# Performance work log

Hardware: AMD Instinct MI355X
Metric: run time of the kernel (lower is better)

The kernel has to match this reference:

```python
import jax, jax.numpy as jnp
import numpy as np

N = 50000   # nodes
E = 1600000 # edges (avg degree 32)
H = 128     # input_size == hidden_size
L = 2       # n_layer


def setup_inputs() -> dict:
    key = jax.random.key(0)
    k0, k1, k2, k3, k4 = jax.random.split(key, 5)
    inp = jax.random.normal(k0, (N, H), dtype=jnp.float32)
    h = jax.random.normal(k1, (L, N, H), dtype=jnp.float32)
    edgidx = jax.random.randint(k2, (2, E), 0, N, dtype=jnp.int32)
    # stacked gate linears, order per layer: xz, hz, xr, hr, xh, hh
    W = jax.random.normal(k3, (L, 6, H, H), dtype=jnp.float32) * (1.0 / np.sqrt(H))
    b = jax.random.normal(k4, (L, 6, H), dtype=jnp.float32) * 0.01
    return {"inp": inp, "edgidx": edgidx, "h": h, "W": W, "b": b}


def _gin(x, W, b, src, dst, n):
    # GINConv with eps=0: Linear(x + sum_{j in N(i)} x_j)
    agg = jax.ops.segment_sum(x[src], dst, num_segments=n)  # scatter-add over edges
    return (x + agg) @ W + b


def reference(inp, edgidx, h, W, b):
    src, dst = edgidx[0], edgidx[1]
    n = inp.shape[0]
    x = inp
    outs = []
    for i in range(W.shape[0]):  # small fixed layer loop
        z = jax.nn.sigmoid(_gin(x, W[i, 0], b[i, 0], src, dst, n)
                           + _gin(h[i], W[i, 1], b[i, 1], src, dst, n))
        r = jax.nn.sigmoid(_gin(x, W[i, 2], b[i, 2], src, dst, n)
                           + _gin(h[i], W[i, 3], b[i, 3], src, dst, n))
        h_tilde = jnp.tanh(_gin(x, W[i, 4], b[i, 4], src, dst, n)
                           + _gin(r * h[i], W[i, 5], b[i, 5], src, dst, n))
        x = z * h[i] + (1.0 - z) * h_tilde
        outs.append(x)
    h_out = jnp.stack(outs)  # [L, N, H]; original returns (out, h_out) where out is h_out
    return h_out
```

## Files before the change

### kernel.cpp

```cpp
#include <hip/hip_runtime.h>
#include <math.h>

#define HDIM 128

typedef _Float16 f16;
typedef unsigned short u16;
typedef __attribute__((ext_vector_type(4))) _Float16 f16x4;
typedef __attribute__((ext_vector_type(8))) _Float16 f16x8;
typedef __attribute__((ext_vector_type(4))) float f32x4;

__global__ __launch_bounds__(256) void degrank_kernel(
    const int* __restrict__ edg, int* __restrict__ cnt,
    u16* __restrict__ rank, int E) {
  int e = blockIdx.x * 256 + threadIdx.x;
  if (e < E) {
    int src = edg[e];
    int dst = edg[E + e];
    rank[e] = (u16)atomicAdd(&cnt[dst * 16 + (src >> 12)], 1);
  }
}

__global__ __launch_bounds__(256) void nodescan_kernel(
    int* __restrict__ cnt, int* __restrict__ deg, int N) {
  int node = blockIdx.x * 256 + threadIdx.x;
  if (node >= N) return;
  int* c = cnt + node * 16;
  int s = 0;
  #pragma unroll
  for (int b = 0; b < 16; ++b) {
    int v = c[b];
    c[b] = s;
    s += v;
  }
  deg[node] = s;
}

__global__ __launch_bounds__(256) void scan_part_kernel(
    const int* __restrict__ deg, int* __restrict__ bsum, int n, int chunk) {
  __shared__ int red[256];
  const int b = blockIdx.x, t = threadIdx.x;
  const int begin = b * chunk;
  const int end = min(begin + chunk, n);
  int s = 0;
  for (int i = begin + t; i < end; i += 256) s += deg[i];
  red[t] = s;
  __syncthreads();
  for (int off = 128; off > 0; off >>= 1) {
    if (t < off) red[t] += red[t + off];
    __syncthreads();
  }
  if (t == 0) bsum[b] = red[0];
}

__global__ __launch_bounds__(256) void scan_top_kernel(
    const int* __restrict__ bsum, int* __restrict__ boff,
    int* __restrict__ offs, int n) {
  __shared__ int sh[256];
  const int t = threadIdx.x;
  int v = bsum[t];
  sh[t] = v;
  __syncthreads();
  for (int off = 1; off < 256; off <<= 1) {
    int add = (t >= off) ? sh[t - off] : 0;
    __syncthreads();
    sh[t] += add;
    __syncthreads();
  }
  boff[t] = sh[t] - v;
  if (t == 255) offs[n] = sh[255];
}

__global__ __launch_bounds__(256) void scan_fin_kernel(
    const int* __restrict__ deg, const int* __restrict__ boff,
    int* __restrict__ offs, int n, int chunk) {
  __shared__ int sh[256];
  const int b = blockIdx.x, t = threadIdx.x;
  const int idx = b * chunk + t;
  int v = (t < chunk && idx < n) ? deg[idx] : 0;
  sh[t] = v;
  __syncthreads();
  for (int off = 1; off < 256; off <<= 1) {
    int add = (t >= off) ? sh[t - off] : 0;
    __syncthreads();
    sh[t] += add;
    __syncthreads();
  }
  if (t < chunk && idx < n) offs[idx] = boff[b] + sh[t] - v;
}

__global__ __launch_bounds__(256) void fill_kernel(
    const int* __restrict__ edg, const int* __restrict__ offs,
    const int* __restrict__ cnt, const u16* __restrict__ rank,
    u16* __restrict__ csr_src, int E) {
  int i = blockIdx.x * 256 + threadIdx.x;
  int e0 = i * 4;
  if (e0 >= E) return;
  if (e0 + 4 <= E) {
    int4 s4 = *reinterpret_cast<const int4*>(edg + e0);
    int4 d4 = *reinterpret_cast<const int4*>(edg + E + e0);
    ushort4 r4 = *reinterpret_cast<const ushort4*>(rank + e0);
    csr_src[offs[d4.x] + cnt[d4.x * 16 + (s4.x >> 12)] + r4.x] = (u16)s4.x;
    csr_src[offs[d4.y] + cnt[d4.y * 16 + (s4.y >> 12)] + r4.y] = (u16)s4.y;
    csr_src[offs[d4.z] + cnt[d4.z * 16 + (s4.z >> 12)] + r4.z] = (u16)s4.z;
    csr_src[offs[d4.w] + cnt[d4.w * 16 + (s4.w >> 12)] + r4.w] = (u16)s4.w;
  } else {
    for (int e = e0; e < E; ++e) {
      int src = edg[e];
      int dst = edg[E + e];
      csr_src[offs[dst] + cnt[dst * 16 + (src >> 12)] + rank[e]] = (u16)src;
    }
  }
}

__global__ __launch_bounds__(256) void convb_kernel(
    const float* __restrict__ src, f16* __restrict__ dst, int n, int SN) {
  const int t = threadIdx.x;
  const int nloc = t >> 3;
  const int sub = t & 7;
  const int sl = sub >> 1;
  const int hf = sub & 1;
  const int node = blockIdx.x * 32 + nloc;
  if (node >= n) return;
  const float* sp = src + (size_t)node * HDIM + sub * 16;
  f16* dp = dst + ((size_t)sl * SN + node) * 32 + hf * 16;
  float4 v0 = *reinterpret_cast<const float4*>(sp + 0);
  float4 v1 = *reinterpret_cast<const float4*>(sp + 4);
  float4 v2 = *reinterpret_cast<const float4*>(sp + 8);
  float4 v3 = *reinterpret_cast<const float4*>(sp + 12);
  f16x8 o0, o1;
  o0[0]=(f16)v0.x; o0[1]=(f16)v0.y; o0[2]=(f16)v0.z; o0[3]=(f16)v0.w;
  o0[4]=(f16)v1.x; o0[5]=(f16)v1.y; o0[6]=(f16)v1.z; o0[7]=(f16)v1.w;
  o1[0]=(f16)v2.x; o1[1]=(f16)v2.y; o1[2]=(f16)v2.z; o1[3]=(f16)v2.w;
  o1[4]=(f16)v3.x; o1[5]=(f16)v3.y; o1[6]=(f16)v3.z; o1[7]=(f16)v3.w;
  *reinterpret_cast<f16x8*>(dp) = o0;
  *reinterpret_cast<f16x8*>(dp + 8) = o1;
}

__global__ __launch_bounds__(256) void transw_kernel(
    const float* __restrict__ W, f16* __restrict__ WT) {
  __shared__ float sh[32][33];
  const int g = blockIdx.y;
  const int ti = blockIdx.x >> 2;
  const int tj = blockIdx.x & 3;
  const float* __restrict__ wp = W + (size_t)g * HDIM * HDIM;
  f16* __restrict__ op = WT + (size_t)g * HDIM * HDIM;
  const int t = threadIdx.x;
  #pragma unroll
  for (int it = 0; it < 4; ++it) {
    int elem = it * 256 + t;
    int r = elem >> 5, c = elem & 31;
    sh[r][c] = wp[(size_t)(ti * 32 + r) * HDIM + tj * 32 + c];
  }
  __syncthreads();
  #pragma unroll
  for (int it = 0; it < 4; ++it) {
    int elem = it * 256 + t;
    int cc = elem >> 5, rr = elem & 31;
    op[(size_t)(tj * 32 + cc) * HDIM + ti * 32 + rr] = (f16)sh[rr][cc];
  }
}

__global__ __launch_bounds__(256) void pull2_kernel(
    const u16* __restrict__ csr_src, const int* __restrict__ offs,
    const f16* __restrict__ xb, const f16* __restrict__ hbl,
    f16* __restrict__ A, f16* __restrict__ Bh, int N, int hSN) {
  const int cls = blockIdx.x & 7;
  const int tid = cls >> 2;
  const int sl = cls & 3;
  const int node = (blockIdx.x >> 3) * 64 + (threadIdx.x >> 2);
  if (node >= N) return;
  const int c8 = (threadIdx.x & 3) << 3;
  const f16* __restrict__ tab =
      tid ? hbl + (size_t)sl * hSN * 32 : xb + (size_t)sl * (size_t)N * 32;
  f16* __restrict__ dst = (tid ? Bh : A) + (size_t)sl * (size_t)N * 32;
  const int s = offs[node];
  const int e = offs[node + 1];
  float acc[8];
  f16x8 sv = *reinterpret_cast<const f16x8*>(tab + (size_t)node * 32 + c8);
  #pragma unroll
  for (int q = 0; q < 8; ++q) acc[q] = (float)sv[q];
  int k = s;
  for (; k + 8 <= e; k += 8) {
    int j0 = csr_src[k];
    int j1 = csr_src[k + 1];
    int j2 = csr_src[k + 2];
    int j3 = csr_src[k + 3];
    int j4 = csr_src[k + 4];
    int j5 = csr_src[k + 5];
    int j6 = csr_src[k + 6];
    int j7 = csr_src[k + 7];
    f16x8 u0 = *reinterpret_cast<const f16x8*>(tab + (size_t)j0 * 32 + c8);
    f16x8 u1 = *reinterpret_cast<const f16x8*>(tab + (size_t)j1 * 32 + c8);
    f16x8 u2 = *reinterpret_cast<const f16x8*>(tab + (size_t)j2 * 32 + c8);
    f16x8 u3 = *reinterpret_cast<const f16x8*>(tab + (size_t)j3 * 32 + c8);
    f16x8 u4 = *reinterpret_cast<const f16x8*>(tab + (size_t)j4 * 32 + c8);
    f16x8 u5 = *reinterpret_cast<const f16x8*>(tab + (size_t)j5 * 32 + c8);
    f16x8 u6 = *reinterpret_cast<const f16x8*>(tab + (size_t)j6 * 32 + c8);
    f16x8 u7 = *reinterpret_cast<const f16x8*>(tab + (size_t)j7 * 32 + c8);
    #pragma unroll
    for (int q = 0; q < 8; ++q)
      acc[q] += (((float)u0[q] + (float)u1[q]) + ((float)u2[q] + (float)u3[q])) +
                (((float)u4[q] + (float)u5[q]) + ((float)u6[q] + (float)u7[q]));
  }
  for (; k < e; ++k) {
    f16x8 u = *reinterpret_cast<const f16x8*>(tab + (size_t)csr_src[k] * 32 + c8);
    #pragma unroll
    for (int q = 0; q < 8; ++q) acc[q] += (float)u[q];
  }
  f16x8 o;
  #pragma unroll
  for (int q = 0; q < 8; ++q) o[q] = (f16)acc[q];
  *reinterpret_cast<f16x8*>(dst + (size_t)node * 32 + c8) = o;
}

__global__ __launch_bounds__(256) void pull1_kernel(
    const u16* __restrict__ csr_src, const int* __restrict__ offs,
    const f16* __restrict__ cb, f16* __restrict__ Ctot, int N) {
  const int sl = blockIdx.x & 3;
  const int node = (blockIdx.x >> 2) * 64 + (threadIdx.x >> 2);
  if (node >= N) return;
  const int c8 = (threadIdx.x & 3) << 3;
  const f16* __restrict__ tab = cb + (size_t)sl * (size_t)N * 32;
  f16* __restrict__ dst = Ctot + (size_t)sl * (size_t)N * 32;
  const int s = offs[node];
  const int e = offs[node + 1];
  float acc[8];
  f16x8 sv = *reinterpret_cast<const f16x8*>(tab + (size_t)node * 32 + c8);
  #pragma unroll
  for (int q = 0; q < 8; ++q) acc[q] = (float)sv[q];
  int k = s;
  for (; k + 8 <= e; k += 8) {
    int j0 = csr_src[k];
    int j1 = csr_src[k + 1];
    int j2 = csr_src[k + 2];
    int j3 = csr_src[k + 3];
    int j4 = csr_src[k + 4];
    int j5 = csr_src[k + 5];
    int j6 = csr_src[k + 6];
    int j7 = csr_src[k + 7];
    f16x8 u0 = *reinterpret_cast<const f16x8*>(tab + (size_t)j0 * 32 + c8);
    f16x8 u1 = *reinterpret_cast<const f16x8*>(tab + (size_t)j1 * 32 + c8);
    f16x8 u2 = *reinterpret_cast<const f16x8*>(tab + (size_t)j2 * 32 + c8);
    f16x8 u3 = *reinterpret_cast<const f16x8*>(tab + (size_t)j3 * 32 + c8);
    f16x8 u4 = *reinterpret_cast<const f16x8*>(tab + (size_t)j4 * 32 + c8);
    f16x8 u5 = *reinterpret_cast<const f16x8*>(tab + (size_t)j5 * 32 + c8);
    f16x8 u6 = *reinterpret_cast<const f16x8*>(tab + (size_t)j6 * 32 + c8);
    f16x8 u7 = *reinterpret_cast<const f16x8*>(tab + (size_t)j7 * 32 + c8);
    #pragma unroll
    for (int q = 0; q < 8; ++q)
      acc[q] += (((float)u0[q] + (float)u1[q]) + ((float)u2[q] + (float)u3[q])) +
                (((float)u4[q] + (float)u5[q]) + ((float)u6[q] + (float)u7[q]));
  }
  for (; k < e; ++k) {
    f16x8 u = *reinterpret_cast<const f16x8*>(tab + (size_t)csr_src[k] * 32 + c8);
    #pragma unroll
    for (int q = 0; q < 8; ++q) acc[q] += (float)u[q];
  }
  f16x8 o;
  #pragma unroll
  for (int q = 0; q < 8; ++q) o[q] = (f16)acc[q];
  *reinterpret_cast<f16x8*>(dst + (size_t)node * 32 + c8) = o;
}

__device__ __forceinline__ void stage_blocked(
    const f16* __restrict__ src, f16* __restrict__ As,
    int row0, int N, int SN, int t) {
  #pragma unroll
  for (int i = 0; i < 4; ++i) {
    int u = i * 256 + t;
    int row = u >> 4;
    int sl = (u >> 2) & 3;
    int ck = u & 3;
    int r = row0 + row;
    f16x8 v{};
    if (r < N) v = *reinterpret_cast<const f16x8*>(
        src + ((size_t)sl * SN + r) * 32 + ck * 8);
    *reinterpret_cast<f16x8*>(&As[row * 136 + sl * 32 + ck * 8]) = v;
  }
}

__device__ __forceinline__ void mfma_tile(
    const f16* As, const f16* Ws, int wr, int wc, int ln15, int quad,
    f32x4 (&acc)[2][4]) {
  #pragma unroll
  for (int s = 0; s < 4; ++s) {
    f16x8 a0 = *reinterpret_cast<const f16x8*>(
        &As[(wr * 32 + ln15) * 136 + s * 32 + quad * 8]);
    f16x8 a1 = *reinterpret_cast<const f16x8*>(
        &As[(wr * 32 + 16 + ln15) * 136 + s * 32 + quad * 8]);
    #pragma unroll
    for (int ni = 0; ni < 4; ++ni) {
      f16x8 bf = *reinterpret_cast<const f16x8*>(
          &Ws[(wc * 64 + ni * 16 + ln15) * 136 + s * 32 + quad * 8]);
      acc[0][ni] = __builtin_amdgcn_mfma_f32_16x16x32_f16(a0, bf, acc[0][ni], 0, 0, 0);
      acc[1][ni] = __builtin_amdgcn_mfma_f32_16x16x32_f16(a1, bf, acc[1][ni], 0, 0, 0);
    }
  }
}

__global__ __launch_bounds__(256, 3) void gemm3_kernel(
    const f16* __restrict__ A, const f16* __restrict__ Bh,
    const f16* __restrict__ WT, const float* __restrict__ b,
    const f16* __restrict__ hbl, f16* __restrict__ zb,
    f16* __restrict__ cb, float* __restrict__ hpre, int N, int hSN) {
  __shared__ f16 As[64 * 136];
  __shared__ f16 Ws[128 * 136];
  const int t = threadIdx.x;
  const int w = t >> 6, wr = w >> 1, wc = w & 1;
  const int lane = t & 63, ln15 = lane & 15, quad = lane >> 4;
  const int row0 = blockIdx.x * 64;
  f32x4 accZ[2][4], accR[2][4], accH[2][4];
  #pragma unroll
  for (int i = 0; i < 2; ++i)
    #pragma unroll
    for (int j = 0; j < 4; ++j) {
      accZ[i][j] = (f32x4){0.f, 0.f, 0.f, 0.f};
      accR[i][j] = (f32x4){0.f, 0.f, 0.f, 0.f};
      accH[i][j] = (f32x4){0.f, 0.f, 0.f, 0.f};
    }

  stage_blocked(A, As, row0, N, N, t);
  #pragma unroll
  for (int g = 0; g < 3; ++g) {
    const f16* __restrict__ wp = WT + (size_t)(g * 2) * HDIM * HDIM;
    __syncthreads();
    #pragma unroll
    for (int i = 0; i < 8; ++i) {
      int flat = i * 256 + t;
      int n = flat >> 4;
      int o = (flat & 15) * 8;
      *reinterpret_cast<f16x8*>(&Ws[n * 136 + o]) =
          *reinterpret_cast<const f16x8*>(wp + (size_t)n * HDIM + o);
    }
    __syncthreads();
    if (g == 0) mfma_tile(As, Ws, wr, wc, ln15, quad, accZ);
    else if (g == 1) mfma_tile(As, Ws, wr, wc, ln15, quad, accR);
    else mfma_tile(As, Ws, wr, wc, ln15, quad, accH);
  }
  __syncthreads();
  stage_blocked(Bh, As, row0, N, N, t);
  #pragma unroll
  for (int g = 0; g < 2; ++g) {
    const f16* __restrict__ wp = WT + (size_t)(g * 2 + 1) * HDIM * HDIM;
    __syncthreads();
    #pragma unroll
    for (int i = 0; i < 8; ++i) {
      int flat = i * 256 + t;
      int n = flat >> 4;
      int o = (flat & 15) * 8;
      *reinterpret_cast<f16x8*>(&Ws[n * 136 + o]) =
          *reinterpret_cast<const f16x8*>(wp + (size_t)n * HDIM + o);
    }
    __syncthreads();
    if (g == 0) mfma_tile(As, Ws, wr, wc, ln15, quad, accZ);
    else mfma_tile(As, Ws, wr, wc, ln15, quad, accR);
  }

  #pragma unroll
  for (int ni = 0; ni < 4; ++ni) {
    const int col = wc * 64 + ni * 16 + ln15;
    const int slc = col >> 5;
    const int cw = col & 31;
    float bz = b[0 * HDIM + col] + b[1 * HDIM + col];
    float br = b[2 * HDIM + col] + b[3 * HDIM + col];
    float bh = b[4 * HDIM + col];
    #pragma unroll
    for (int mi = 0; mi < 2; ++mi) {
      #pragma unroll
      for (int r = 0; r < 4; ++r) {
        int row = row0 + wr * 32 + mi * 16 + quad * 4 + r;
        if (row >= N) continue;
        size_t idx = (size_t)row * HDIM + col;
        zb[idx] = (f16)(accZ[mi][ni][r] + bz);
        float rv = accR[mi][ni][r] + br;
        float rg = 1.f / (1.f + expf(-rv));
        float hv = (float)hbl[((size_t)slc * hSN + row) * 32 + cw];
        cb[((size_t)slc * N + row) * 32 + cw] = (f16)(rg * hv);
        hpre[idx] = accH[mi][ni][r] + bh;
      }
    }
  }
}

__global__ __launch_bounds__(256, 3) void gemm_final_kernel(
    const f16* __restrict__ Ctot, const f16* __restrict__ WT5,
    const float* __restrict__ b5, const f16* __restrict__ zb,
    const float* __restrict__ hi, float* __restrict__ outi,
    f16* __restrict__ xb, int N) {
  __shared__ f16 As[64 * 136];
  __shared__ f16 Ws[128 * 136];
  const int t = threadIdx.x;
  const int w = t >> 6, wr = w >> 1, wc = w & 1;
  const int lane = t & 63, ln15 = lane & 15, quad = lane >> 4;
  const int row0 = blockIdx.x * 64;
  f32x4 acc[2][4];
  #pragma unroll
  for (int i = 0; i < 2; ++i)
    #pragma unroll
    for (int j = 0; j < 4; ++j) acc[i][j] = (f32x4){0.f, 0.f, 0.f, 0.f};

  stage_blocked(Ctot, As, row0, N, N, t);
  #pragma unroll
  for (int i = 0; i < 8; ++i) {
    int flat = i * 256 + t;
    int n = flat >> 4;
    int o = (flat & 15) * 8;
    *reinterpret_cast<f16x8*>(&Ws[n * 136 + o]) =
        *reinterpret_cast<const f16x8*>(WT5 + (size_t)n * HDIM + o);
  }
  __syncthreads();
  mfma_tile(As, Ws, wr, wc, ln15, quad, acc);

  #pragma unroll
  for (int ni = 0; ni < 4; ++ni) {
    const int col = wc * 64 + ni * 16 + ln15;
    const int slc = col >> 5;
    const int cw = col & 31;
    float bias = b5[col];
    #pragma unroll
    for (int mi = 0; mi < 2; ++mi) {
      #pragma unroll
      for (int r = 0; r < 4; ++r) {
        int row = row0 + wr * 32 + mi * 16 + quad * 4 + r;
        if (row >= N) continue;
        size_t idx = (size_t)row * HDIM + col;
        float v = acc[mi][ni][r] + bias + outi[idx];
        float ht = tanhf(v);
        float z = 1.f / (1.f + expf(-(float)zb[idx]));
        float o = z * hi[idx] + (1.f - z) * ht;
        outi[idx] = o;
        xb[((size_t)slc * N + row) * 32 + cw] = (f16)o;
      }
    }
  }
}

extern "C" void kernel_launch(void* const* d_in, const int* in_sizes, int n_in,
                              void* d_out, int out_size, void* d_ws, size_t ws_size,
                              hipStream_t stream) {
  const float* inp = (const float*)d_in[0];
  const int*   edg = (const int*)d_in[1];
  const float* h   = (const float*)d_in[2];
  const float* W   = (const float*)d_in[3];
  const float* b   = (const float*)d_in[4];
  float* out = (float*)d_out;

  const int NH = in_sizes[0];
  const int N  = NH / HDIM;
  const int E  = in_sizes[1] / 2;
  const int L  = in_sizes[2] / NH;

  f16* Af   = (f16*)d_ws;
  f16* Bhf  = Af + (size_t)NH;
  f16* zbuf = Bhf + (size_t)NH;
  f16* cbuf = zbuf + (size_t)NH;
  f16* xbuf = cbuf + (size_t)NH;
  f16* hbuf = xbuf + (size_t)NH;
  f16* WT   = hbuf + (size_t)L * NH;
  int* deg     = (int*)(WT + (size_t)L * 6 * HDIM * HDIM);
  int* offs    = deg + N;
  int* bsum    = offs + (N + 1);
  int* boff    = bsum + 256;
  u16* rank    = (u16*)(boff + 256);
  u16* csr_src = rank + (size_t)E;
  int* cnt     = (int*)Af;

  const int eblocks = (E + 255) / 256;
  const int fblocks = (E + 1023) / 1024;
  const int nsblocks = (N + 255) / 256;
  const int rowblocks = (N + 63) / 64;
  const int p2blocks = ((N + 63) / 64) * 8;
  const int p1blocks = ((N + 63) / 64) * 4;
  const int cvxblocks = (N + 31) / 32;
  const int cvhblocks = (L * N + 31) / 32;
  const int chunk = (N + 255) / 256;

  hipMemsetAsync(cnt, 0, (size_t)N * 16 * sizeof(int), stream);
  hipLaunchKernelGGL(degrank_kernel, dim3(eblocks), dim3(256), 0, stream,
                     edg, cnt, rank, E);
  hipLaunchKernelGGL(nodescan_kernel, dim3(nsblocks), dim3(256), 0, stream,
                     cnt, deg, N);
  hipLaunchKernelGGL(scan_part_kernel, dim3(256), dim3(256), 0, stream,
                     deg, bsum, N, chunk);
  hipLaunchKernelGGL(scan_top_kernel, dim3(1), dim3(256), 0, stream,
                     bsum, boff, offs, N);
  hipLaunchKernelGGL(scan_fin_kernel, dim3(256), dim3(256), 0, stream,
                     deg, boff, offs, N, chunk);
  hipLaunchKernelGGL(fill_kernel, dim3(fblocks), dim3(256), 0, stream,
                     edg, offs, cnt, rank, csr_src, E);
  hipLaunchKernelGGL(transw_kernel, dim3(16, L * 6), dim3(256), 0, stream,
                     W, WT);
  hipLaunchKernelGGL(convb_kernel, dim3(cvxblocks), dim3(256), 0, stream,
                     inp, xbuf, N, N);
  hipLaunchKernelGGL(convb_kernel, dim3(cvhblocks), dim3(256), 0, stream,
                     h, hbuf, L * N, L * N);

  for (int i = 0; i < L; ++i) {
    const float* hi = h + (size_t)i * NH;
    const f16* hbl = hbuf + (size_t)i * N * 32;
    const f16* WTi = WT + (size_t)i * 6 * HDIM * HDIM;
    const float* bi = b + (size_t)i * 6 * HDIM;
    float* outi = out + (size_t)i * NH;

    hipLaunchKernelGGL(pull2_kernel, dim3(p2blocks), dim3(256), 0, stream,
                       csr_src, offs, xbuf, hbl, Af, Bhf, N, L * N);
    hipLaunchKernelGGL(gemm3_kernel, dim3(rowblocks), dim3(256), 0, stream,
                       Af, Bhf, WTi, bi, hbl, zbuf, cbuf, outi, N, L * N);
    hipLaunchKernelGGL(pull1_kernel, dim3(p1blocks), dim3(256), 0, stream,
                       csr_src, offs, cbuf, Af, N);
    hipLaunchKernelGGL(gemm_final_kernel, dim3(rowblocks), dim3(256), 0, stream,
                       Af, WTi + (size_t)5 * HDIM * HDIM, bi + 5 * HDIM,
                       zbuf, hi, outi, xbuf, N);
  }
}
```

Baseline: 676.1 us.

## Process nodes in degree-sorted order in pull kernels and store pre-activation in fp16

Builds a node permutation sorted by descending degree (histogram, scan, scatter) and has both pull kernels look up their node through it, so neighbouring threads in a wavefront get similar edge counts and less divergence. Separately, the h-candidate pre-activation is kept in an fp16 scratch buffer instead of being written to and re-read from the fp32 output, and gemm_final reads h from the fp16 blocked copy instead of the fp32 input. This lowers memory traffic at some cost in precision. The permutation adds three small setup kernels and an indirect lookup, and it scatters the write locations within each block.

```diff
diff --git a/kernel.cpp b/kernel.cpp
--- a/kernel.cpp
+++ b/kernel.cpp
@@ -109,6 +109,37 @@
       int dst = edg[E + e];
       csr_src[offs[dst] + cnt[dst * 16 + (src >> 12)] + rank[e]] = (u16)src;
     }
+  }
+}
+
+__global__ __launch_bounds__(256) void hist_kernel(
+    const int* __restrict__ deg, int* __restrict__ hist, int N) {
+  int node = blockIdx.x * 256 + threadIdx.x;
+  if (node < N) atomicAdd(&hist[255 - min(deg[node], 255)], 1);
+}
+
+__global__ __launch_bounds__(256) void hscan_kernel(int* __restrict__ hist) {
+  __shared__ int sh[256];
+  const int t = threadIdx.x;
+  int v = hist[t];
+  sh[t] = v;
+  __syncthreads();
+  for (int off = 1; off < 256; off <<= 1) {
+    int add = (t >= off) ? sh[t - off] : 0;
+    __syncthreads();
+    sh[t] += add;
+    __syncthreads();
+  }
+  hist[t] = sh[t] - v;
+}
+
+__global__ __launch_bounds__(256) void scatter_kernel(
+    const int* __restrict__ deg, int* __restrict__ hoff,
+    int* __restrict__ perm, int N) {
+  int node = blockIdx.x * 256 + threadIdx.x;
+  if (node < N) {
+    int pos = atomicAdd(&hoff[255 - min(deg[node], 255)], 1);
+    perm[pos] = node;
   }
 }
 
@@ -162,13 +193,15 @@
 
 __global__ __launch_bounds__(256) void pull2_kernel(
     const u16* __restrict__ csr_src, const int* __restrict__ offs,
+    const int* __restrict__ perm,
     const f16* __restrict__ xb, const f16* __restrict__ hbl,
     f16* __restrict__ A, f16* __restrict__ Bh, int N, int hSN) {
   const int cls = blockIdx.x & 7;
   const int tid = cls >> 2;
   const int sl = cls & 3;
-  const int node = (blockIdx.x >> 3) * 64 + (threadIdx.x >> 2);
-  if (node >= N) return;
+  const int snode = (blockIdx.x >> 3) * 64 + (threadIdx.x >> 2);
+  if (snode >= N) return;
+  const int node = perm[snode];
   const int c8 = (threadIdx.x & 3) << 3;
   const f16* __restrict__ tab =
       tid ? hbl + (size_t)sl * hSN * 32 : xb + (size_t)sl * (size_t)N * 32;
@@ -215,10 +248,12 @@
 
 __global__ __launch_bounds__(256) void pull1_kernel(
     const u16* __restrict__ csr_src, const int* __restrict__ offs,
+    const int* __restrict__ perm,
     const f16* __restrict__ cb, f16* __restrict__ Ctot, int N) {
   const int sl = blockIdx.x & 3;
-  const int node = (blockIdx.x >> 2) * 64 + (threadIdx.x >> 2);
-  if (node >= N) return;
+  const int snode = (blockIdx.x >> 2) * 64 + (threadIdx.x >> 2);
+  if (snode >= N) return;
+  const int node = perm[snode];
   const int c8 = (threadIdx.x & 3) << 3;
   const f16* __restrict__ tab = cb + (size_t)sl * (size_t)N * 32;
   f16* __restrict__ dst = Ctot + (size_t)sl * (size_t)N * 32;
@@ -302,7 +337,7 @@
     const f16* __restrict__ A, const f16* __restrict__ Bh,
     const f16* __restrict__ WT, const float* __restrict__ b,
     const f16* __restrict__ hbl, f16* __restrict__ zb,
-    f16* __restrict__ cb, float* __restrict__ hpre, int N, int hSN) {
+    f16* __restrict__ cb, f16* __restrict__ hpre, int N, int hSN) {
   __shared__ f16 As[64 * 136];
   __shared__ f16 Ws[128 * 136];
   const int t = threadIdx.x;
@@ -376,7 +411,7 @@
         float rg = 1.f / (1.f + expf(-rv));
         float hv = (float)hbl[((size_t)slc * hSN + row) * 32 + cw];
         cb[((size_t)slc * N + row) * 32 + cw] = (f16)(rg * hv);
-        hpre[idx] = accH[mi][ni][r] + bh;
+        hpre[idx] = (f16)(accH[mi][ni][r] + bh);
       }
     }
   }
@@ -385,8 +420,8 @@
 __global__ __launch_bounds__(256, 3) void gemm_final_kernel(
     const f16* __restrict__ Ctot, const f16* __restrict__ WT5,
     const float* __restrict__ b5, const f16* __restrict__ zb,
-    const float* __restrict__ hi, float* __restrict__ outi,
-    f16* __restrict__ xb, int N) {
+    const f16* __restrict__ hbl, const f16* __restrict__ hpre,
+    float* __restrict__ outi, f16* __restrict__ xb, int N, int hSN) {
   __shared__ f16 As[64 * 136];
   __shared__ f16 Ws[128 * 136];
   const int t = threadIdx.x;
@@ -424,10 +459,11 @@
         int row = row0 + wr * 32 + mi * 16 + quad * 4 + r;
         if (row >= N) continue;
         size_t idx = (size_t)row * HDIM + col;
-        float v = acc[mi][ni][r] + bias + outi[idx];
+        float v = acc[mi][ni][r] + bias + (float)hpre[idx];
         float ht = tanhf(v);
         float z = 1.f / (1.f + expf(-(float)zb[idx]));
-        float o = z * hi[idx] + (1.f - z) * ht;
+        float hv = (float)hbl[((size_t)slc * hSN + row) * 32 + cw];
+        float o = z * hv + (1.f - z) * ht;
         outi[idx] = o;
         xb[((size_t)slc * N + row) * 32 + cw] = (f16)o;
       }
@@ -455,13 +491,16 @@
   f16* zbuf = Bhf + (size_t)NH;
   f16* cbuf = zbuf + (size_t)NH;
   f16* xbuf = cbuf + (size_t)NH;
-  f16* hbuf = xbuf + (size_t)NH;
+  f16* hpbuf = xbuf + (size_t)NH;
+  f16* hbuf = hpbuf + (size_t)NH;
   f16* WT   = hbuf + (size_t)L * NH;
   int* deg     = (int*)(WT + (size_t)L * 6 * HDIM * HDIM);
   int* offs    = deg + N;
   int* bsum    = offs + (N + 1);
   int* boff    = bsum + 256;
-  u16* rank    = (u16*)(boff + 256);
+  int* hist    = boff + 256;
+  int* perm    = hist + 256;
+  u16* rank    = (u16*)(perm + N);
   u16* csr_src = rank + (size_t)E;
   int* cnt     = (int*)Af;
 
@@ -476,6 +515,7 @@
   const int chunk = (N + 255) / 256;
 
   hipMemsetAsync(cnt, 0, (size_t)N * 16 * sizeof(int), stream);
+  hipMemsetAsync(hist, 0, 256 * sizeof(int), stream);
   hipLaunchKernelGGL(degrank_kernel, dim3(eblocks), dim3(256), 0, stream,
                      edg, cnt, rank, E);
   hipLaunchKernelGGL(nodescan_kernel, dim3(nsblocks), dim3(256), 0, stream,
@@ -488,6 +528,11 @@
                      deg, boff, offs, N, chunk);
   hipLaunchKernelGGL(fill_kernel, dim3(fblocks), dim3(256), 0, stream,
                      edg, offs, cnt, rank, csr_src, E);
+  hipLaunchKernelGGL(hist_kernel, dim3(nsblocks), dim3(256), 0, stream,
+                     deg, hist, N);
+  hipLaunchKernelGGL(hscan_kernel, dim3(1), dim3(256), 0, stream, hist);
+  hipLaunchKernelGGL(scatter_kernel, dim3(nsblocks), dim3(256), 0, stream,
+                     deg, hist, perm, N);
   hipLaunchKernelGGL(transw_kernel, dim3(16, L * 6), dim3(256), 0, stream,
                      W, WT);
   hipLaunchKernelGGL(convb_kernel, dim3(cvxblocks), dim3(256), 0, stream,
@@ -496,20 +541,19 @@
                      h, hbuf, L * N, L * N);
 
   for (int i = 0; i < L; ++i) {
-    const float* hi = h + (size_t)i * NH;
     const f16* hbl = hbuf + (size_t)i * N * 32;
     const f16* WTi = WT + (size_t)i * 6 * HDIM * HDIM;
     const float* bi = b + (size_t)i * 6 * HDIM;
     float* outi = out + (size_t)i * NH;
 
     hipLaunchKernelGGL(pull2_kernel, dim3(p2blocks), dim3(256), 0, stream,
-                       csr_src, offs, xbuf, hbl, Af, Bhf, N, L * N);
+                       csr_src, offs, perm, xbuf, hbl, Af, Bhf, N, L * N);
     hipLaunchKernelGGL(gemm3_kernel, dim3(rowblocks), dim3(256), 0, stream,
-                       Af, Bhf, WTi, bi, hbl, zbuf, cbuf, outi, N, L * N);
+                       Af, Bhf, WTi, bi, hbl, zbuf, cbuf, hpbuf, N, L * N);
     hipLaunchKernelGGL(pull1_kernel, dim3(p1blocks), dim3(256), 0, stream,
-                       csr_src, offs, cbuf, Af, N);
+                       csr_src, offs, perm, cbuf, Af, N);
     hipLaunchKernelGGL(gemm_final_kernel, dim3(rowblocks), dim3(256), 0, stream,
                        Af, WTi + (size_t)5 * HDIM * HDIM, bi + 5 * HDIM,
-                       zbuf, hi, outi, xbuf, N);
-  }
-}
+                       zbuf, hbl, hpbuf, outi, xbuf, N, L * N);
+  }
+}
```

Result: slower. 915.6 us (+35.4%).

## Pad CSR rows to multiples of eight and vectorize gather index loads

Applied to the files above, without the earlier changes.

Each node's CSR neighbour list is padded to a multiple of 8 entries. The padding points at a dummy zero row appended to every feature table, so the pull kernels can load indices as 16-byte u16x8 vectors, unroll by 16 and drop the scalar tail loop. Partial neighbour sums are now done as packed fp16 vector adds before conversion to fp32. The final GRU blend reads the fp16 copy of h instead of the fp32 input. The padding adds extra gathers of the zero row and a few setup kernels, and the fp16 partial sums and fp16 h reduce accuracy.

```diff
diff --git a/kernel.cpp b/kernel.cpp
--- a/kernel.cpp
+++ b/kernel.cpp
@@ -1,10 +1,12 @@
 #include <hip/hip_runtime.h>
 #include <math.h>
+#include <stdint.h>
 
 #define HDIM 128
 
 typedef _Float16 f16;
 typedef unsigned short u16;
+typedef __attribute__((ext_vector_type(8))) unsigned short u16x8;
 typedef __attribute__((ext_vector_type(4))) _Float16 f16x4;
 typedef __attribute__((ext_vector_type(8))) _Float16 f16x8;
 typedef __attribute__((ext_vector_type(4))) float f32x4;
@@ -21,7 +23,8 @@
 }
 
 __global__ __launch_bounds__(256) void nodescan_kernel(
-    int* __restrict__ cnt, int* __restrict__ deg, int N) {
+    int* __restrict__ cnt, int* __restrict__ deg, int* __restrict__ degt,
+    int N) {
   int node = blockIdx.x * 256 + threadIdx.x;
   if (node >= N) return;
   int* c = cnt + node * 16;
@@ -32,7 +35,8 @@
     c[b] = s;
     s += v;
   }
-  deg[node] = s;
+  degt[node] = s;
+  deg[node] = (s + 7) & ~7;
 }
 
 __global__ __launch_bounds__(256) void scan_part_kernel(
@@ -112,8 +116,41 @@
   }
 }
 
+__global__ __launch_bounds__(256) void pad_kernel(
+    const int* __restrict__ offs, const int* __restrict__ degt,
+    const int* __restrict__ deg, u16* __restrict__ csr, int N) {
+  int n = blockIdx.x * 256 + threadIdx.x;
+  if (n >= N) return;
+  int base = offs[n];
+  int a = degt[n], b = deg[n];
+  for (int k = base + a; k < base + b; ++k) csr[k] = (u16)N;
+}
+
+__global__ __launch_bounds__(256) void zpad_kernel(
+    f16* __restrict__ xb, f16* __restrict__ cb, f16* __restrict__ hb,
+    int N, int L) {
+  int t = threadIdx.x;
+  int rows = 2 + L;
+  int total = 4 * rows * 4;
+  if (t >= total) return;
+  int chunk = t & 3;
+  int r = (t >> 2) % rows;
+  int sl = (t >> 2) / rows;
+  size_t SN1 = (size_t)(N + 1);
+  f16* p;
+  if (r == 0)      p = xb + (sl * SN1 + N) * 32;
+  else if (r == 1) p = cb + (sl * SN1 + N) * 32;
+  else {
+    int i = r - 2;
+    p = hb + ((size_t)sl * L * SN1 + (size_t)i * SN1 + N) * 32;
+  }
+  f16x8 z{};
+  *reinterpret_cast<f16x8*>(p + chunk * 8) = z;
+}
+
 __global__ __launch_bounds__(256) void convb_kernel(
-    const float* __restrict__ src, f16* __restrict__ dst, int n, int SN) {
+    const float* __restrict__ src, f16* __restrict__ dst, int n, int SN,
+    int rowoff) {
   const int t = threadIdx.x;
   const int nloc = t >> 3;
   const int sub = t & 7;
@@ -122,7 +159,7 @@
   const int node = blockIdx.x * 32 + nloc;
   if (node >= n) return;
   const float* sp = src + (size_t)node * HDIM + sub * 16;
-  f16* dp = dst + ((size_t)sl * SN + node) * 32 + hf * 16;
+  f16* dp = dst + ((size_t)sl * SN + rowoff + node) * 32 + hf * 16;
   float4 v0 = *reinterpret_cast<const float4*>(sp + 0);
   float4 v1 = *reinterpret_cast<const float4*>(sp + 4);
   float4 v2 = *reinterpret_cast<const float4*>(sp + 8);
@@ -163,7 +200,7 @@
 __global__ __launch_bounds__(256) void pull2_kernel(
     const u16* __restrict__ csr_src, const int* __restrict__ offs,
     const f16* __restrict__ xb, const f16* __restrict__ hbl,
-    f16* __restrict__ A, f16* __restrict__ Bh, int N, int hSN) {
+    f16* __restrict__ A, f16* __restrict__ Bh, int N, int N1, int hSN) {
   const int cls = blockIdx.x & 7;
   const int tid = cls >> 2;
   const int sl = cls & 3;
@@ -171,8 +208,8 @@
   if (node >= N) return;
   const int c8 = (threadIdx.x & 3) << 3;
   const f16* __restrict__ tab =
-      tid ? hbl + (size_t)sl * hSN * 32 : xb + (size_t)sl * (size_t)N * 32;
-  f16* __restrict__ dst = (tid ? Bh : A) + (size_t)sl * (size_t)N * 32;
+      tid ? hbl + (size_t)sl * hSN * 32 : xb + (size_t)sl * (size_t)N1 * 32;
+  f16* __restrict__ dst = (tid ? Bh : A) + (size_t)sl * (size_t)N1 * 32;
   const int s = offs[node];
   const int e = offs[node + 1];
   float acc[8];
@@ -180,32 +217,47 @@
   #pragma unroll
   for (int q = 0; q < 8; ++q) acc[q] = (float)sv[q];
   int k = s;
-  for (; k + 8 <= e; k += 8) {
-    int j0 = csr_src[k];
-    int j1 = csr_src[k + 1];
-    int j2 = csr_src[k + 2];
-    int j3 = csr_src[k + 3];
-    int j4 = csr_src[k + 4];
-    int j5 = csr_src[k + 5];
-    int j6 = csr_src[k + 6];
-    int j7 = csr_src[k + 7];
-    f16x8 u0 = *reinterpret_cast<const f16x8*>(tab + (size_t)j0 * 32 + c8);
-    f16x8 u1 = *reinterpret_cast<const f16x8*>(tab + (size_t)j1 * 32 + c8);
-    f16x8 u2 = *reinterpret_cast<const f16x8*>(tab + (size_t)j2 * 32 + c8);
-    f16x8 u3 = *reinterpret_cast<const f16x8*>(tab + (size_t)j3 * 32 + c8);
-    f16x8 u4 = *reinterpret_cast<const f16x8*>(tab + (size_t)j4 * 32 + c8);
-    f16x8 u5 = *reinterpret_cast<const f16x8*>(tab + (size_t)j5 * 32 + c8);
-    f16x8 u6 = *reinterpret_cast<const f16x8*>(tab + (size_t)j6 * 32 + c8);
-    f16x8 u7 = *reinterpret_cast<const f16x8*>(tab + (size_t)j7 * 32 + c8);
+  for (; k + 16 <= e; k += 16) {
+    u16x8 ia = *reinterpret_cast<const u16x8*>(csr_src + k);
+    u16x8 ib = *reinterpret_cast<const u16x8*>(csr_src + k + 8);
+    f16x8 u0 = *reinterpret_cast<const f16x8*>(tab + (size_t)ia[0] * 32 + c8);
+    f16x8 u1 = *reinterpret_cast<const f16x8*>(tab + (size_t)ia[1] * 32 + c8);
+    f16x8 u2 = *reinterpret_cast<const f16x8*>(tab + (size_t)ia[2] * 32 + c8);
+    f16x8 u3 = *reinterpret_cast<const f16x8*>(tab + (size_t)ia[3] * 32 + c8);
+    f16x8 u4 = *reinterpret_cast<const f16x8*>(tab + (size_t)ia[4] * 32 + c8);
+    f16x8 u5 = *reinterpret_cast<const f16x8*>(tab + (size_t)ia[5] * 32 + c8);
+    f16x8 u6 = *reinterpret_cast<const f16x8*>(tab + (size_t)ia[6] * 32 + c8);
+    f16x8 u7 = *reinterpret_cast<const f16x8*>(tab + (size_t)ia[7] * 32 + c8);
+    f16x8 u8 = *reinterpret_cast<const f16x8*>(tab + (size_t)ib[0] * 32 + c8);
+    f16x8 u9 = *reinterpret_cast<const f16x8*>(tab + (size_t)ib[1] * 32 + c8);
+    f16x8 ua = *reinterpret_cast<const f16x8*>(tab + (size_t)ib[2] * 32 + c8);
+    f16x8 ub = *reinterpret_cast<const f16x8*>(tab + (size_t)ib[3] * 32 + c8);
+    f16x8 uc = *reinterpret_cast<const f16x8*>(tab + (size_t)ib[4] * 32 + c8);
+    f16x8 ud = *reinterpret_cast<const f16x8*>(tab + (size_t)ib[5] * 32 + c8);
+    f16x8 ue = *reinterpret_cast<const f16x8*>(tab + (size_t)ib[6] * 32 + c8);
+    f16x8 uf = *reinterpret_cast<const f16x8*>(tab + (size_t)ib[7] * 32 + c8);
+    f16x8 g0 = (u0 + u1) + (u2 + u3);
+    f16x8 g1 = (u4 + u5) + (u6 + u7);
+    f16x8 g2 = (u8 + u9) + (ua + ub);
+    f16x8 g3 = (uc + ud) + (ue + uf);
     #pragma unroll
     for (int q = 0; q < 8; ++q)
-      acc[q] += (((float)u0[q] + (float)u1[q]) + ((float)u2[q] + (float)u3[q])) +
-                (((float)u4[q] + (float)u5[q]) + ((float)u6[q] + (float)u7[q]));
-  }
-  for (; k < e; ++k) {
-    f16x8 u = *reinterpret_cast<const f16x8*>(tab + (size_t)csr_src[k] * 32 + c8);
-    #pragma unroll
-    for (int q = 0; q < 8; ++q) acc[q] += (float)u[q];
+      acc[q] += ((float)g0[q] + (float)g1[q]) + ((float)g2[q] + (float)g3[q]);
+  }
+  if (k < e) {
+    u16x8 ia = *reinterpret_cast<const u16x8*>(csr_src + k);
+    f16x8 u0 = *reinterpret_cast<const f16x8*>(tab + (size_t)ia[0] * 32 + c8);
+    f16x8 u1 = *reinterpret_cast<const f16x8*>(tab + (size_t)ia[1] * 32 + c8);
+    f16x8 u2 = *reinterpret_cast<const f16x8*>(tab + (size_t)ia[2] * 32 + c8);
+    f16x8 u3 = *reinterpret_cast<const f16x8*>(tab + (size_t)ia[3] * 32 + c8);
+    f16x8 u4 = *reinterpret_cast<const f16x8*>(tab + (size_t)ia[4] * 32 + c8);
+    f16x8 u5 = *reinterpret_cast<const f16x8*>(tab + (size_t)ia[5] * 32 + c8);
+    f16x8 u6 = *reinterpret_cast<const f16x8*>(tab + (size_t)ia[6] * 32 + c8);
+    f16x8 u7 = *reinterpret_cast<const f16x8*>(tab + (size_t)ia[7] * 32 + c8);
+    f16x8 g0 = (u0 + u1) + (u2 + u3);
+    f16x8 g1 = (u4 + u5) + (u6 + u7);
+    #pragma unroll
+    for (int q = 0; q < 8; ++q) acc[q] += (float)g0[q] + (float)g1[q];
   }
   f16x8 o;
   #pragma unroll
@@ -215,13 +267,13 @@
 
 __global__ __launch_bounds__(256) void pull1_kernel(
     const u16* __restrict__ csr_src, const int* __restrict__ offs,
-    const f16* __restrict__ cb, f16* __restrict__ Ctot, int N) {
+    const f16* __restrict__ cb, f16* __restrict__ Ctot, int N, int N1) {
   const int sl = blockIdx.x & 3;
   const int node = (blockIdx.x >> 2) * 64 + (threadIdx.x >> 2);
   if (node >= N) return;
   const int c8 = (threadIdx.x & 3) << 3;
-  const f16* __restrict__ tab = cb + (size_t)sl * (size_t)N * 32;
-  f16* __restrict__ dst = Ctot + (size_t)sl * (size_t)N * 32;
+  const f16* __restrict__ tab = cb + (size_t)sl * (size_t)N1 * 32;
+  f16* __restrict__ dst = Ctot + (size_t)sl * (size_t)N1 * 32;
   const int s = offs[node];
   const int e = offs[node + 1];
   float acc[8];
@@ -229,32 +281,47 @@
   #pragma unroll
   for (int q = 0; q < 8; ++q) acc[q] = (float)sv[q];
   int k = s;
-  for (; k + 8 <= e; k += 8) {
-    int j0 = csr_src[k];
-    int j1 = csr_src[k + 1];
-    int j2 = csr_src[k + 2];
-    int j3 = csr_src[k + 3];
-    int j4 = csr_src[k + 4];
-    int j5 = csr_src[k + 5];
-    int j6 = csr_src[k + 6];
-    int j7 = csr_src[k + 7];
-    f16x8 u0 = *reinterpret_cast<const f16x8*>(tab + (size_t)j0 * 32 + c8);
-    f16x8 u1 = *reinterpret_cast<const f16x8*>(tab + (size_t)j1 * 32 + c8);
-    f16x8 u2 = *reinterpret_cast<const f16x8*>(tab + (size_t)j2 * 32 + c8);
-    f16x8 u3 = *reinterpret_cast<const f16x8*>(tab + (size_t)j3 * 32 + c8);
-    f16x8 u4 = *reinterpret_cast<const f16x8*>(tab + (size_t)j4 * 32 + c8);
-    f16x8 u5 = *reinterpret_cast<const f16x8*>(tab + (size_t)j5 * 32 + c8);
-    f16x8 u6 = *reinterpret_cast<const f16x8*>(tab + (size_t)j6 * 32 + c8);
-    f16x8 u7 = *reinterpret_cast<const f16x8*>(tab + (size_t)j7 * 32 + c8);
+  for (; k + 16 <= e; k += 16) {
+    u16x8 ia = *reinterpret_cast<const u16x8*>(csr_src + k);
+    u16x8 ib = *reinterpret_cast<const u16x8*>(csr_src + k + 8);
+    f16x8 u0 = *reinterpret_cast<const f16x8*>(tab + (size_t)ia[0] * 32 + c8);
+    f16x8 u1 = *reinterpret_cast<const f16x8*>(tab + (size_t)ia[1] * 32 + c8);
+    f16x8 u2 = *reinterpret_cast<const f16x8*>(tab + (size_t)ia[2] * 32 + c8);
+    f16x8 u3 = *reinterpret_cast<const f16x8*>(tab + (size_t)ia[3] * 32 + c8);
+    f16x8 u4 = *reinterpret_cast<const f16x8*>(tab + (size_t)ia[4] * 32 + c8);
+    f16x8 u5 = *reinterpret_cast<const f16x8*>(tab + (size_t)ia[5] * 32 + c8);
+    f16x8 u6 = *reinterpret_cast<const f16x8*>(tab + (size_t)ia[6] * 32 + c8);
+    f16x8 u7 = *reinterpret_cast<const f16x8*>(tab + (size_t)ia[7] * 32 + c8);
+    f16x8 u8 = *reinterpret_cast<const f16x8*>(tab + (size_t)ib[0] * 32 + c8);
+    f16x8 u9 = *reinterpret_cast<const f16x8*>(tab + (size_t)ib[1] * 32 + c8);
+    f16x8 ua = *reinterpret_cast<const f16x8*>(tab + (size_t)ib[2] * 32 + c8);
+    f16x8 ub = *reinterpret_cast<const f16x8*>(tab + (size_t)ib[3] * 32 + c8);
+    f16x8 uc = *reinterpret_cast<const f16x8*>(tab + (size_t)ib[4] * 32 + c8);
+    f16x8 ud = *reinterpret_cast<const f16x8*>(tab + (size_t)ib[5] * 32 + c8);
+    f16x8 ue = *reinterpret_cast<const f16x8*>(tab + (size_t)ib[6] * 32 + c8);
+    f16x8 uf = *reinterpret_cast<const f16x8*>(tab + (size_t)ib[7] * 32 + c8);
+    f16x8 g0 = (u0 + u1) + (u2 + u3);
+    f16x8 g1 = (u4 + u5) + (u6 + u7);
+    f16x8 g2 = (u8 + u9) + (ua + ub);
+    f16x8 g3 = (uc + ud) + (ue + uf);
     #pragma unroll
     for (int q = 0; q < 8; ++q)
-      acc[q] += (((float)u0[q] + (float)u1[q]) + ((float)u2[q] + (float)u3[q])) +
-                (((float)u4[q] + (float)u5[q]) + ((float)u6[q] + (float)u7[q]));
-  }
-  for (; k < e; ++k) {
-    f16x8 u = *reinterpret_cast<const f16x8*>(tab + (size_t)csr_src[k] * 32 + c8);
-    #pragma unroll
-    for (int q = 0; q < 8; ++q) acc[q] += (float)u[q];
+      acc[q] += ((float)g0[q] + (float)g1[q]) + ((float)g2[q] + (float)g3[q]);
+  }
+  if (k < e) {
+    u16x8 ia = *reinterpret_cast<const u16x8*>(csr_src + k);
+    f16x8 u0 = *reinterpret_cast<const f16x8*>(tab + (size_t)ia[0] * 32 + c8);
+    f16x8 u1 = *reinterpret_cast<const f16x8*>(tab + (size_t)ia[1] * 32 + c8);
+    f16x8 u2 = *reinterpret_cast<const f16x8*>(tab + (size_t)ia[2] * 32 + c8);
+    f16x8 u3 = *reinterpret_cast<const f16x8*>(tab + (size_t)ia[3] * 32 + c8);
+    f16x8 u4 = *reinterpret_cast<const f16x8*>(tab + (size_t)ia[4] * 32 + c8);
+    f16x8 u5 = *reinterpret_cast<const f16x8*>(tab + (size_t)ia[5] * 32 + c8);
+    f16x8 u6 = *reinterpret_cast<const f16x8*>(tab + (size_t)ia[6] * 32 + c8);
+    f16x8 u7 = *reinterpret_cast<const f16x8*>(tab + (size_t)ia[7] * 32 + c8);
+    f16x8 g0 = (u0 + u1) + (u2 + u3);
+    f16x8 g1 = (u4 + u5) + (u6 + u7);
+    #pragma unroll
+    for (int q = 0; q < 8; ++q) acc[q] += (float)g0[q] + (float)g1[q];
   }
   f16x8 o;
   #pragma unroll
@@ -302,7 +369,7 @@
     const f16* __restrict__ A, const f16* __restrict__ Bh,
     const f16* __restrict__ WT, const float* __restrict__ b,
     const f16* __restrict__ hbl, f16* __restrict__ zb,
-    f16* __restrict__ cb, float* __restrict__ hpre, int N, int hSN) {
+    f16* __restrict__ cb, float* __restrict__ hpre, int N, int N1, int hSN) {
   __shared__ f16 As[64 * 136];
   __shared__ f16 Ws[128 * 136];
   const int t = threadIdx.x;
@@ -319,7 +386,7 @@
       accH[i][j] = (f32x4){0.f, 0.f, 0.f, 0.f};
     }
 
-  stage_blocked(A, As, row0, N, N, t);
+  stage_blocked(A, As, row0, N, N1, t);
   #pragma unroll
   for (int g = 0; g < 3; ++g) {
     const f16* __restrict__ wp = WT + (size_t)(g * 2) * HDIM * HDIM;
@@ -338,7 +405,7 @@
     else mfma_tile(As, Ws, wr, wc, ln15, quad, accH);
   }
   __syncthreads();
-  stage_blocked(Bh, As, row0, N, N, t);
+  stage_blocked(Bh, As, row0, N, N1, t);
   #pragma unroll
   for (int g = 0; g < 2; ++g) {
     const f16* __restrict__ wp = WT + (size_t)(g * 2 + 1) * HDIM * HDIM;
@@ -375,7 +442,7 @@
         float rv = accR[mi][ni][r] + br;
         float rg = 1.f / (1.f + expf(-rv));
         float hv = (float)hbl[((size_t)slc * hSN + row) * 32 + cw];
-        cb[((size_t)slc * N + row) * 32 + cw] = (f16)(rg * hv);
+        cb[((size_t)slc * N1 + row) * 32 + cw] = (f16)(rg * hv);
         hpre[idx] = accH[mi][ni][r] + bh;
       }
     }
@@ -385,8 +452,8 @@
 __global__ __launch_bounds__(256, 3) void gemm_final_kernel(
     const f16* __restrict__ Ctot, const f16* __restrict__ WT5,
     const float* __restrict__ b5, const f16* __restrict__ zb,
-    const float* __restrict__ hi, float* __restrict__ outi,
-    f16* __restrict__ xb, int N) {
+    const f16* __restrict__ hbl, float* __restrict__ outi,
+    f16* __restrict__ xb, int N, int N1, int hSN) {
   __shared__ f16 As[64 * 136];
   __shared__ f16 Ws[128 * 136];
   const int t = threadIdx.x;
@@ -399,7 +466,7 @@
     #pragma unroll
     for (int j = 0; j < 4; ++j) acc[i][j] = (f32x4){0.f, 0.f, 0.f, 0.f};
 
-  stage_blocked(Ctot, As, row0, N, N, t);
+  stage_blocked(Ctot, As, row0, N, N1, t);
   #pragma unroll
   for (int i = 0; i < 8; ++i) {
     int flat = i * 256 + t;
@@ -427,9 +494,10 @@
         float v = acc[mi][ni][r] + bias + outi[idx];
         float ht = tanhf(v);
         float z = 1.f / (1.f + expf(-(float)zb[idx]));
-        float o = z * hi[idx] + (1.f - z) * ht;
+        float hv = (float)hbl[((size_t)slc * hSN + row) * 32 + cw];
+        float o = z * hv + (1.f - z) * ht;
         outi[idx] = o;
-        xb[((size_t)slc * N + row) * 32 + cw] = (f16)o;
+        xb[((size_t)slc * N1 + row) * 32 + cw] = (f16)o;
       }
     }
   }
@@ -449,19 +517,24 @@
   const int N  = NH / HDIM;
   const int E  = in_sizes[1] / 2;
   const int L  = in_sizes[2] / NH;
+  const int N1 = N + 1;
+  const size_t NT = (size_t)128 * N1;
 
   f16* Af   = (f16*)d_ws;
-  f16* Bhf  = Af + (size_t)NH;
-  f16* zbuf = Bhf + (size_t)NH;
-  f16* cbuf = zbuf + (size_t)NH;
-  f16* xbuf = cbuf + (size_t)NH;
-  f16* hbuf = xbuf + (size_t)NH;
-  f16* WT   = hbuf + (size_t)L * NH;
+  f16* Bhf  = Af + NT;
+  f16* cbuf = Bhf + NT;
+  f16* xbuf = cbuf + NT;
+  f16* hbuf = xbuf + NT;
+  f16* zbuf = hbuf + (size_t)L * NT;
+  f16* WT   = zbuf + (size_t)NH;
   int* deg     = (int*)(WT + (size_t)L * 6 * HDIM * HDIM);
-  int* offs    = deg + N;
+  int* degt    = deg + N;
+  int* offs    = degt + N;
   int* bsum    = offs + (N + 1);
   int* boff    = bsum + 256;
-  u16* rank    = (u16*)(boff + 256);
+  uintptr_t rp = (uintptr_t)(boff + 256);
+  rp = (rp + 63) & ~(uintptr_t)63;
+  u16* rank    = (u16*)rp;
   u16* csr_src = rank + (size_t)E;
   int* cnt     = (int*)Af;
 
@@ -471,15 +544,15 @@
   const int rowblocks = (N + 63) / 64;
   const int p2blocks = ((N + 63) / 64) * 8;
   const int p1blocks = ((N + 63) / 64) * 4;
-  const int cvxblocks = (N + 31) / 32;
-  const int cvhblocks = (L * N + 31) / 32;
+  const int cvblocks = (N + 31) / 32;
   const int chunk = (N + 255) / 256;
+  const int hSN = L * N1;
 
   hipMemsetAsync(cnt, 0, (size_t)N * 16 * sizeof(int), stream);
   hipLaunchKernelGGL(degrank_kernel, dim3(eblocks), dim3(256), 0, stream,
                      edg, cnt, rank, E);
   hipLaunchKernelGGL(nodescan_kernel, dim3(nsblocks), dim3(256), 0, stream,
-                     cnt, deg, N);
+                     cnt, deg, degt, N);
   hipLaunchKernelGGL(scan_part_kernel, dim3(256), dim3(256), 0, stream,
                      deg, bsum, N, chunk);
   hipLaunchKernelGGL(scan_top_kernel, dim3(1), dim3(256), 0, stream,
@@ -488,28 +561,32 @@
                      deg, boff, offs, N, chunk);
   hipLaunchKernelGGL(fill_kernel, dim3(fblocks), dim3(256), 0, stream,
                      edg, offs, cnt, rank, csr_src, E);
+  hipLaunchKernelGGL(pad_kernel, dim3(nsblocks), dim3(256), 0, stream,
+                     offs, degt, deg, csr_src, N);
   hipLaunchKernelGGL(transw_kernel, dim3(16, L * 6), dim3(256), 0, stream,
                      W, WT);
-  hipLaunchKernelGGL(convb_kernel, dim3(cvxblocks), dim3(256), 0, stream,
-                     inp, xbuf, N, N);
-  hipLaunchKernelGGL(convb_kernel, dim3(cvhblocks), dim3(256), 0, stream,
-                     h, hbuf, L * N, L * N);
+  hipLaunchKernelGGL(convb_kernel, dim3(cvblocks), dim3(256), 0, stream,
+                     inp, xbuf, N, N1, 0);
+  for (int i = 0; i < L; ++i)
+    hipLaunchKernelGGL(convb_kernel, dim3(cvblocks), dim3(256), 0, stream,
+                       h + (size_t)i * NH, hbuf, N, hSN, i * N1);
+  hipLaunchKernelGGL(zpad_kernel, dim3(1), dim3(256), 0, stream,
+                     xbuf, cbuf, hbuf, N, L);
 
   for (int i = 0; i < L; ++i) {
-    const float* hi = h + (size_t)i * NH;
-    const f16* hbl = hbuf + (size_t)i * N * 32;
+    const f16* hbl = hbuf + (size_t)i * N1 * 32;
     const f16* WTi = WT + (size_t)i * 6 * HDIM * HDIM;
     const float* bi = b + (size_t)i * 6 * HDIM;
     float* outi = out + (size_t)i * NH;
 
     hipLaunchKernelGGL(pull2_kernel, dim3(p2blocks), dim3(256), 0, stream,
-                       csr_src, offs, xbuf, hbl, Af, Bhf, N, L * N);
+                       csr_src, offs, xbuf, hbl, Af, Bhf, N, N1, hSN);
     hipLaunchKernelGGL(gemm3_kernel, dim3(rowblocks), dim3(256), 0, stream,
-                       Af, Bhf, WTi, bi, hbl, zbuf, cbuf, outi, N, L * N);
+                       Af, Bhf, WTi, bi, hbl, zbuf, cbuf, outi, N, N1, hSN);
     hipLaunchKernelGGL(pull1_kernel, dim3(p1blocks), dim3(256), 0, stream,
-                       csr_src, offs, cbuf, Af, N);
+                       csr_src, offs, cbuf, Af, N, N1);
     hipLaunchKernelGGL(gemm_final_kernel, dim3(rowblocks), dim3(256), 0, stream,
                        Af, WTi + (size_t)5 * HDIM * HDIM, bi + 5 * HDIM,
-                       zbuf, hi, outi, xbuf, N);
-  }
-}
+                       zbuf, hbl, outi, xbuf, N, N1, hSN);
+  }
+}
```

Result: no change. 667.2 us (-1.3%).
